# Optimization experiments

Measured on AMD Instinct MI355X. Metric: run time of the kernel, lower is better.

## Reference

```python
import jax, jax.numpy as jnp
import numpy as np

B, NP1, D = 64, 1025, 256  # N+1 tokens, feature dim d (label dim makes d+1)
N_LAYER, N_HEAD = 4, 4
VAR = 0.02


def _pad_pq(allparam):
    """Build padded (d+1)x(d+1) P_full/Q_full for all layers/heads at once.
    P_full gets a 1 at [d, d]; Q_full is zero-padded."""
    L, H, _, d, _ = allparam.shape
    Pf = (jnp.zeros((L, H, d + 1, d + 1), allparam.dtype)
          .at[:, :, :d, :d].set(allparam[:, :, 0])
          .at[:, :, d, d].set(1.0))
    Qf = (jnp.zeros((L, H, d + 1, d + 1), allparam.dtype)
          .at[:, :, :d, :d].set(allparam[:, :, 1]))
    return Pf, Qf


def setup_inputs() -> dict:
    key = jax.random.key(0)
    k1, k2 = jax.random.split(key)
    Z = jax.random.normal(k1, (B, NP1, D + 1), dtype=jnp.float32)
    allparam = jax.random.normal(k2, (N_LAYER, N_HEAD, 2, D, D), dtype=jnp.float32) * VAR
    return {"Z": Z, "allparam": allparam}


def reference(Z, allparam):
    Bb, Np1, dp1 = Z.shape
    N = Np1 - 1
    Pf, Qf = _pad_pq(allparam)  # (L, H, d+1, d+1)
    # mask A = diag(1,...,1,0): equivalent to zeroing the last key token
    mask = jnp.ones((Np1,), Z.dtype).at[N].set(0.0)
    for l in range(allparam.shape[0]):
        # attn[b,h,n,m] = Z[b,n,:] @ Q_full[h] @ Z[b,m,:]
        attn = jnp.einsum('bni,hij,bmj->bhnm', Z, Qf[l], Z)
        attn = jax.nn.relu(attn)
        # key[b,h,m,i] = P_full[h] @ Z[b,m,:], last token masked out (A matrix)
        key_t = jnp.einsum('hij,bmj->bhmi', Pf[l], Z) * mask[None, None, :, None]
        # sum over heads fused into the einsum reduction; scale by 1/N
        res = jnp.einsum('bhnm,bhmi->bni', attn, key_t) / N
        Z = Z + res  # residual connection
    return Z
```

## Files before the change

### kernel.cpp

```cpp
#include <hip/hip_runtime.h>
#include <cstdint>
#include <cstddef>

#define B_    64
#define NP1   1025
#define N_    1024
#define D_    256
#define DP1   257
#define L_    4
#define H_    4
#define MT    1024
#define NCHE  32
#define IPAD  272
#define TR_   1024

typedef __bf16 bf16;
typedef bf16 bf16x4 __attribute__((ext_vector_type(4)));
typedef bf16 bf16x8 __attribute__((ext_vector_type(8)));
typedef float f32x4 __attribute__((ext_vector_type(4)));

__device__ __forceinline__ f32x4 mfma16(bf16x8 a, bf16x8 b, f32x4 c) {
    return __builtin_amdgcn_mfma_f32_16x16x32_bf16(a, b, c, 0, 0, 0);
}

__device__ __forceinline__ void async16(const void* g, void* l) {
    __builtin_amdgcn_global_load_lds(
        (const __attribute__((address_space(1))) void*)g,
        (__attribute__((address_space(3))) void*)l, 16, 0, 0);
}

__global__ void k_prep_pq(const float* __restrict__ ap,
                          bf16* __restrict__ Pb, bf16* __restrict__ Qt) {
    int idx = blockIdx.x * 256 + threadIdx.x;
    int j  = idx & 255;
    int i  = (idx >> 8) & 255;
    int lh = idx >> 16;
    const float* base = ap + (size_t)lh * 2 * D_ * D_;
    float p = base[i * D_ + j];
    float q = base[D_ * D_ + i * D_ + j];
    Pb[((size_t)lh * D_ + i) * D_ + j] = (bf16)p;
    Qt[((size_t)lh * D_ + j) * D_ + i] = (bf16)q;
}

__global__ __launch_bounds__(256) void k_zbt(const float* __restrict__ Z,
                                             bf16* __restrict__ Zb,
                                             bf16* __restrict__ ZbT) {
    __shared__ float t[64][65];
    int m0 = blockIdx.x * 64, j0 = blockIdx.y * 64, b = blockIdx.z;
    int c = threadIdx.x & 63, r0 = threadIdx.x >> 6;
#pragma unroll
    for (int s = 0; s < 16; s++) {
        int r = s * 4 + r0;
        int j = j0 + c;
        float v = (j < DP1) ? Z[((size_t)b * NP1 + m0 + r) * DP1 + j] : 0.f;
        t[r][c] = v;
        if (j < D_) Zb[((size_t)b * N_ + m0 + r) * D_ + j] = (bf16)v;
    }
    __syncthreads();
#pragma unroll
    for (int s = 0; s < 16; s++) {
        int rr = s * 4 + r0;
        int j = j0 + rr;
        if (j < DP1)
            ZbT[((size_t)b * DP1 + j) * MT + m0 + c] = (bf16)t[c][rr];
    }
}

__global__ __launch_bounds__(512, 1) void k_attn(const bf16* __restrict__ Zb,
                                                 const bf16* __restrict__ ZbT,
                                                 const bf16* __restrict__ Qt,
                                                 const bf16* __restrict__ Pb,
                                                 float* __restrict__ Z,
                                                 bf16* __restrict__ T,
                                                 bf16* __restrict__ Tlab,
                                                 int layer) {
    __shared__ bf16 zbS[2][32][256];
    __shared__ bf16 ztS[2][IPAD][32];
    __shared__ bf16 sl[8][32][40];

    const int tid  = threadIdx.x;
    const int id   = blockIdx.x;
    const int wave = tid >> 6, lane = tid & 63;
    const int quad = lane >> 4, l16 = lane & 15;

    if (id >= 256) {
        const int bq = id - 256;
        float* lz1 = (float*)&zbS[0][0][0];
        float* lzq = lz1 + 256;
        float* lsS = lzq + 256;
        float* lT  = lsS + 1024;
        const bf16* Zbb2  = Zb  + (size_t)bq * N_ * D_;
        const bf16* ZbTb2 = ZbT + (size_t)bq * DP1 * MT;
        if (tid < 256) lz1[tid] = Z[((size_t)bq * NP1 + N_) * DP1 + tid];
        float outacc = 0.f, labacc = 0.f;
        __syncthreads();
        for (int h = 0; h < H_; h++) {
            const bf16* Qth = Qt + (size_t)(layer * H_ + h) * D_ * D_;
            const bf16* Ph  = Pb + (size_t)(layer * H_ + h) * D_ * D_;
            if (tid < 256) {
                float a = 0.f;
                const bf16* qr = Qth + (size_t)tid * D_;
                for (int i8 = 0; i8 < 32; i8++) {
                    bf16x8 q = *(const bf16x8*)(qr + i8 * 8);
#pragma unroll
                    for (int k = 0; k < 8; k++) a += lz1[i8 * 8 + k] * (float)q[k];
                }
                lzq[tid] = a;
            }
            __syncthreads();
            for (int m = tid; m < N_; m += 512) {
                float a = 0.f;
                const bf16* zr = Zbb2 + (size_t)m * D_;
                for (int j8 = 0; j8 < 32; j8++) {
                    bf16x8 z8 = *(const bf16x8*)(zr + j8 * 8);
#pragma unroll
                    for (int k = 0; k < 8; k++) a += lzq[j8 * 8 + k] * (float)z8[k];
                }
                lsS[m] = a > 0.f ? a : 0.f;
            }
            __syncthreads();
            if (tid < DP1) {
                float tv = 0.f;
                const bf16* tr2 = ZbTb2 + (size_t)tid * MT;
                for (int m8 = 0; m8 < 128; m8++) {
                    bf16x8 t8 = *(const bf16x8*)(tr2 + m8 * 8);
#pragma unroll
                    for (int k = 0; k < 8; k++) tv += lsS[m8 * 8 + k] * (float)t8[k];
                }
                lT[tid] = tv;
            }
            __syncthreads();
            if (tid < 256) {
                const bf16* pr = Ph + (size_t)tid * D_;
                for (int j8 = 0; j8 < 32; j8++) {
                    bf16x8 p8 = *(const bf16x8*)(pr + j8 * 8);
#pragma unroll
                    for (int k = 0; k < 8; k++) outacc += lT[j8 * 8 + k] * (float)p8[k];
                }
            } else if (tid == 256) {
                labacc += lT[256];
            }
            __syncthreads();
        }
        const float inv = 1.0f / (float)N_;
        if (tid < 256)  Z[((size_t)bq * NP1 + N_) * DP1 + tid] += outacc * inv;
        if (tid == 256) Z[((size_t)bq * NP1 + N_) * DP1 + D_]  += labacc * inv;
        return;
    }

    const int xcd = id & 7, u = id >> 3;
    const int b   = xcd + 8 * (u & 7);
    const int bx  = u >> 3;
    const int n0w = bx * 256 + wave * 32;

    const bf16* Zbb  = Zb  + (size_t)b * N_ * D_;
    const bf16* ZbTb = ZbT + (size_t)b * DP1 * MT;

    const int zrow  = wave * 2 + (lane >> 5);
    const int zscol = ((lane & 31) ^ (zrow & 7)) * 8;
    const int krow  = wave * 16 + (lane >> 2);
    const int kscol = ((lane & 3) ^ ((lane >> 3) & 3)) * 8;
    const int xs    = l16 & 7;
    const int kf    = (l16 >> 1) & 3;

    auto stage = [&](int mc_, int p_) {
        int m0 = mc_ * 32;
        const bf16* zsrc = Zbb + (size_t)(m0 + zrow) * D_ + zscol;
#pragma unroll
        for (int t = 0; t < 2; t++)
            async16(zsrc + (size_t)t * 16 * D_, &zbS[p_][t * 16 + wave * 2][0]);
        const bf16* ksrc = ZbTb + (size_t)krow * MT + m0 + kscol;
#pragma unroll
        for (int t = 0; t < 2; t++)
            async16(ksrc + (size_t)t * 128 * MT, &ztS[p_][t * 128 + wave * 16][0]);
        if (wave == 0)
            async16(ksrc + (size_t)256 * MT, &ztS[p_][256][0]);
    };

    int p = 0;

    for (int h = 0; h < H_; h++) {
        const bf16* Qth = Qt + (size_t)(layer * H_ + h) * D_ * D_;

        if (h == 0) stage(0, 0);

        f32x4 acc[2][17];
#pragma unroll
        for (int ns = 0; ns < 2; ns++)
#pragma unroll
            for (int it = 0; it < 17; it++) acc[ns][it] = (f32x4){0.f, 0.f, 0.f, 0.f};

        bf16x8 zqa[2][8];
#pragma unroll 2
        for (int jc = 0; jc < 8; jc++) {
            f32x4 c00 = (f32x4){0.f,0.f,0.f,0.f}, c01 = c00, c10 = c00, c11 = c00;
#pragma unroll
            for (int kc = 0; kc < 8; kc++) {
                const bf16* qb = Qth + (size_t)(jc * 32 + l16) * D_ + kc * 32 + quad * 8;
                const bf16* az = Zbb + (size_t)(n0w + l16) * D_ + kc * 32 + quad * 8;
                bf16x8 q0 = *(const bf16x8*)(qb);
                bf16x8 q1 = *(const bf16x8*)(qb + 16 * D_);
                bf16x8 a0 = *(const bf16x8*)(az);
                bf16x8 a1 = *(const bf16x8*)(az + 16 * D_);
                c00 = mfma16(q0, a0, c00);
                c01 = mfma16(q0, a1, c01);
                c10 = mfma16(q1, a0, c10);
                c11 = mfma16(q1, a1, c11);
            }
            f32x4 cv[2][2] = {{c00, c01}, {c10, c11}};
#pragma unroll
            for (int jt = 0; jt < 2; jt++)
#pragma unroll
                for (int ns = 0; ns < 2; ns++) {
                    bf16x4 pk;
#pragma unroll
                    for (int r = 0; r < 4; r++) pk[r] = (bf16)cv[jt][ns][r];
                    *(bf16x4*)(&sl[wave][ns * 16 + l16][jt * 16 + quad * 4]) = pk;
                }
#pragma unroll
            for (int ns = 0; ns < 2; ns++)
                zqa[ns][jc] = *(const bf16x8*)(&sl[wave][ns * 16 + l16][quad * 8]);
        }

        if (h == 0) {
            asm volatile("s_waitcnt vmcnt(0)" ::: "memory");
            __builtin_amdgcn_s_barrier();
            __builtin_amdgcn_sched_barrier(0);
        }

        for (int cc = 0; cc < NCHE; cc++) {
            const bool haveNext = (cc + 1 < NCHE);
            if (haveNext) {
                int mcn = (h & 1) ? (NCHE - 2 - cc) : (cc + 1);
                stage(mcn, p ^ 1);
                if (wave == 0) asm volatile("s_waitcnt vmcnt(5)" ::: "memory");
                else           asm volatile("s_waitcnt vmcnt(4)" ::: "memory");
            } else {
                asm volatile("s_waitcnt vmcnt(0)" ::: "memory");
            }
            __builtin_amdgcn_s_barrier();
            __builtin_amdgcn_sched_barrier(0);

#pragma unroll
            for (int mt = 0; mt < 2; mt++) {
                f32x4 st0 = (f32x4){0.f,0.f,0.f,0.f}, st1 = st0;
                const bf16* zr = &zbS[p][mt * 16 + l16][0];
                __builtin_amdgcn_s_setprio(1);
#pragma unroll
                for (int kc = 0; kc < 8; kc++) {
                    bf16x8 az = *(const bf16x8*)(zr + (((kc * 4 + quad) ^ xs) * 8));
                    st0 = mfma16(az, zqa[0][kc], st0);
                    st1 = mfma16(az, zqa[1][kc], st1);
                }
                __builtin_amdgcn_s_setprio(0);
                bf16x4 p0, p1;
#pragma unroll
                for (int r = 0; r < 4; r++) {
                    p0[r] = (bf16)(st0[r] > 0.f ? st0[r] : 0.f);
                    p1[r] = (bf16)(st1[r] > 0.f ? st1[r] : 0.f);
                }
                *(bf16x4*)(&sl[wave][l16][mt * 16 + quad * 4])      = p0;
                *(bf16x4*)(&sl[wave][16 + l16][mt * 16 + quad * 4]) = p1;
            }
            bf16x8 sfrag[2];
#pragma unroll
            for (int ns = 0; ns < 2; ns++)
                sfrag[ns] = *(const bf16x8*)(&sl[wave][ns * 16 + l16][quad * 8]);

            __builtin_amdgcn_s_setprio(1);
#pragma unroll
            for (int it = 0; it < 17; it++) {
                const bf16* kr = &ztS[p][it * 16 + l16][0];
                bf16x8 bk = *(const bf16x8*)(kr + ((quad ^ kf) * 8));
                acc[0][it] = mfma16(sfrag[0], bk, acc[0][it]);
                acc[1][it] = mfma16(sfrag[1], bk, acc[1][it]);
            }
            __builtin_amdgcn_s_setprio(0);

            __builtin_amdgcn_sched_barrier(0);
            __builtin_amdgcn_s_barrier();
            if (haveNext) p ^= 1;
        }

        bf16* Th  = T    + (size_t)(b * H_ + h) * TR_ * D_;
        bf16* Tlh = Tlab + (size_t)(b * H_ + h) * TR_;
#pragma unroll
        for (int ns = 0; ns < 2; ns++)
#pragma unroll
            for (int it = 0; it < 17; it++)
#pragma unroll
                for (int r = 0; r < 4; r++) {
                    int n = n0w + ns * 16 + quad * 4 + r;
                    float v = acc[ns][it][r];
                    if (it < 16)
                        Th[(size_t)n * D_ + it * 16 + l16] = (bf16)v;
                    else if (l16 == 0)
                        Tlh[n] = (bf16)v;
                }
    }
}

__global__ __launch_bounds__(256, 4) void k_post(const bf16* __restrict__ T,
                                                 const bf16* __restrict__ Tlab,
                                                 const bf16* __restrict__ Pb,
                                                 float* __restrict__ Z,
                                                 bf16* __restrict__ Zb,
                                                 bf16* __restrict__ ZbT,
                                                 int layer) {
    const int tid  = threadIdx.x;
    const int id   = blockIdx.x;
    const int wave = tid >> 6, lane = tid & 63;
    const int quad = lane >> 4, l16 = lane & 15;
    const int xcd = id & 7, u = id >> 3;
    const int b   = xcd + 8 * (u & 3) + 32 * ((u >> 5) & 1);
    const int bx  = (u >> 2) & 7;
    const int ih  = u >> 6;
    const int n0w = bx * 128 + wave * 32;
    const int i0  = ih * 128;

    f32x4 acc[2][8];
#pragma unroll
    for (int ns = 0; ns < 2; ns++)
#pragma unroll
        for (int it = 0; it < 8; it++) acc[ns][it] = (f32x4){0.f, 0.f, 0.f, 0.f};

    for (int h = 0; h < H_; h++) {
        const bf16* Th = T  + (size_t)(b * H_ + h) * TR_ * D_;
        const bf16* Ph = Pb + (size_t)(layer * H_ + h) * D_ * D_;
#pragma unroll 2
        for (int kc = 0; kc < 8; kc++) {
            bf16x8 af[2];
#pragma unroll
            for (int ns = 0; ns < 2; ns++) {
                int row = n0w + ns * 16 + l16;
                af[ns] = *(const bf16x8*)(Th + (size_t)row * D_ + kc * 32 + quad * 8);
            }
#pragma unroll
            for (int it = 0; it < 8; it++) {
                bf16x8 bp = *(const bf16x8*)(Ph + (size_t)(i0 + it * 16 + l16) * D_ + kc * 32 + quad * 8);
                acc[0][it] = mfma16(af[0], bp, acc[0][it]);
                acc[1][it] = mfma16(af[1], bp, acc[1][it]);
            }
        }
    }

    const float inv = 1.0f / (float)N_;
    const bool wnext = (layer < L_ - 1);
#pragma unroll
    for (int ns = 0; ns < 2; ns++)
#pragma unroll
        for (int it = 0; it < 8; it++) {
            const int i = i0 + it * 16 + l16;
            const int nbase = n0w + ns * 16 + quad * 4;
            bf16x4 zpk;
#pragma unroll
            for (int r = 0; r < 4; r++) {
                int n = nbase + r;
                size_t zi = ((size_t)b * NP1 + n) * DP1 + i;
                float v = Z[zi] + acc[ns][it][r] * inv;
                Z[zi] = v;
                zpk[r] = (bf16)v;
                if (wnext) Zb[((size_t)b * N_ + n) * D_ + i] = (bf16)v;
            }
            if (wnext)
                *(bf16x4*)(&ZbT[((size_t)b * DP1 + i) * MT + nbase]) = zpk;
        }
    if (ih == 0 && tid < 128) {
        int n = bx * 128 + tid;
        float s = 0.f;
#pragma unroll
        for (int h = 0; h < H_; h++)
            s += (float)Tlab[(size_t)(b * H_ + h) * TR_ + n];
        size_t zi = ((size_t)b * NP1 + n) * DP1 + D_;
        float v = Z[zi] + s * inv;
        Z[zi] = v;
        if (wnext) ZbT[((size_t)b * DP1 + D_) * MT + n] = (bf16)v;
    }
}

extern "C" void kernel_launch(void* const* d_in, const int* in_sizes, int n_in,
                              void* d_out, int out_size, void* d_ws, size_t ws_size,
                              hipStream_t stream) {
    const float* Zin = (const float*)d_in[0];
    const float* ap  = (const float*)d_in[1];
    float* Z = (float*)d_out;

    char* ws = (char*)d_ws;
    const size_t sz_Zb  = (size_t)B_ * N_ * D_ * sizeof(bf16);
    const size_t sz_ZbT = (size_t)B_ * DP1 * MT * sizeof(bf16);
    const size_t sz_T   = (size_t)B_ * H_ * TR_ * D_ * sizeof(bf16);
    const size_t sz_Tl  = (size_t)B_ * H_ * TR_ * sizeof(bf16);
    const size_t sz_P   = (size_t)L_ * H_ * D_ * D_ * sizeof(bf16);
    bf16* Zb  = (bf16*)ws;
    bf16* ZbT = (bf16*)(ws + sz_Zb);
    bf16* Tb  = (bf16*)(ws + sz_Zb + sz_ZbT);
    bf16* Tl  = (bf16*)(ws + sz_Zb + sz_ZbT + sz_T);
    bf16* Pb  = (bf16*)(ws + sz_Zb + sz_ZbT + sz_T + sz_Tl);
    bf16* Qt  = (bf16*)(ws + sz_Zb + sz_ZbT + sz_T + sz_Tl + sz_P);

    hipMemcpyAsync(Z, Zin, (size_t)B_ * NP1 * DP1 * sizeof(float),
                   hipMemcpyDeviceToDevice, stream);

    k_prep_pq<<<dim3((L_ * H_ * D_ * D_) / 256), 256, 0, stream>>>(ap, Pb, Qt);
    k_zbt<<<dim3(N_ / 64, 5, B_), 256, 0, stream>>>(Z, Zb, ZbT);

    for (int l = 0; l < L_; l++) {
        k_attn<<<dim3(320), 512, 0, stream>>>(Zb, ZbT, Qt, Pb, Z, Tb, Tl, l);
        k_post<<<dim3(1024), 256, 0, stream>>>(Tb, Tl, Pb, Z, Zb, ZbT, l);
    }
}
```

Measured before the change: 3.590 ms.

## Fold last-token query work into main attention blocks and batch heads

```diff
diff --git a/kernel.cpp b/kernel.cpp
--- a/kernel.cpp
+++ b/kernel.cpp
@@ -83,71 +83,6 @@
     const int wave = tid >> 6, lane = tid & 63;
     const int quad = lane >> 4, l16 = lane & 15;
 
-    if (id >= 256) {
-        const int bq = id - 256;
-        float* lz1 = (float*)&zbS[0][0][0];
-        float* lzq = lz1 + 256;
-        float* lsS = lzq + 256;
-        float* lT  = lsS + 1024;
-        const bf16* Zbb2  = Zb  + (size_t)bq * N_ * D_;
-        const bf16* ZbTb2 = ZbT + (size_t)bq * DP1 * MT;
-        if (tid < 256) lz1[tid] = Z[((size_t)bq * NP1 + N_) * DP1 + tid];
-        float outacc = 0.f, labacc = 0.f;
-        __syncthreads();
-        for (int h = 0; h < H_; h++) {
-            const bf16* Qth = Qt + (size_t)(layer * H_ + h) * D_ * D_;
-            const bf16* Ph  = Pb + (size_t)(layer * H_ + h) * D_ * D_;
-            if (tid < 256) {
-                float a = 0.f;
-                const bf16* qr = Qth + (size_t)tid * D_;
-                for (int i8 = 0; i8 < 32; i8++) {
-                    bf16x8 q = *(const bf16x8*)(qr + i8 * 8);
-#pragma unroll
-                    for (int k = 0; k < 8; k++) a += lz1[i8 * 8 + k] * (float)q[k];
-                }
-                lzq[tid] = a;
-            }
-            __syncthreads();
-            for (int m = tid; m < N_; m += 512) {
-                float a = 0.f;
-                const bf16* zr = Zbb2 + (size_t)m * D_;
-                for (int j8 = 0; j8 < 32; j8++) {
-                    bf16x8 z8 = *(const bf16x8*)(zr + j8 * 8);
-#pragma unroll
-                    for (int k = 0; k < 8; k++) a += lzq[j8 * 8 + k] * (float)z8[k];
-                }
-                lsS[m] = a > 0.f ? a : 0.f;
-            }
-            __syncthreads();
-            if (tid < DP1) {
-                float tv = 0.f;
-                const bf16* tr2 = ZbTb2 + (size_t)tid * MT;
-                for (int m8 = 0; m8 < 128; m8++) {
-                    bf16x8 t8 = *(const bf16x8*)(tr2 + m8 * 8);
-#pragma unroll
-                    for (int k = 0; k < 8; k++) tv += lsS[m8 * 8 + k] * (float)t8[k];
-                }
-                lT[tid] = tv;
-            }
-            __syncthreads();
-            if (tid < 256) {
-                const bf16* pr = Ph + (size_t)tid * D_;
-                for (int j8 = 0; j8 < 32; j8++) {
-                    bf16x8 p8 = *(const bf16x8*)(pr + j8 * 8);
-#pragma unroll
-                    for (int k = 0; k < 8; k++) outacc += lT[j8 * 8 + k] * (float)p8[k];
-                }
-            } else if (tid == 256) {
-                labacc += lT[256];
-            }
-            __syncthreads();
-        }
-        const float inv = 1.0f / (float)N_;
-        if (tid < 256)  Z[((size_t)bq * NP1 + N_) * DP1 + tid] += outacc * inv;
-        if (tid == 256) Z[((size_t)bq * NP1 + N_) * DP1 + D_]  += labacc * inv;
-        return;
-    }
-
     const int xcd = id & 7, u = id >> 3;
     const int b   = xcd + 8 * (u & 7);
     const int bx  = u >> 3;
@@ -297,6 +232,86 @@
                     else if (l16 == 0)
                         Tlh[n] = (bf16)v;
                 }
+    }
+
+    if (bx == 0) {
+        __syncthreads();
+        float* lz1 = (float*)&zbS[0][0][0];
+        float* lzq = lz1 + 256;
+        float* lsS = lzq + 1024;
+        float* lT  = lsS + 4096;
+        if (tid < 256) lz1[tid] = Z[((size_t)b * NP1 + N_) * DP1 + tid];
+        __syncthreads();
+        {
+            int j = tid & 255, hh = tid >> 8;
+            for (int h2 = hh; h2 < H_; h2 += 2) {
+                const bf16* qr = Qt + ((size_t)(layer * H_ + h2) * D_ + j) * D_;
+                float a = 0.f;
+                for (int i8 = 0; i8 < 32; i8++) {
+                    bf16x8 q = *(const bf16x8*)(qr + i8 * 8);
+#pragma unroll
+                    for (int k = 0; k < 8; k++) a += lz1[i8 * 8 + k] * (float)q[k];
+                }
+                lzq[h2 * 256 + j] = a;
+            }
+        }
+        __syncthreads();
+        for (int m = tid; m < N_; m += 512) {
+            const bf16* zr = Zbb + (size_t)m * D_;
+            float a0 = 0.f, a1 = 0.f, a2 = 0.f, a3 = 0.f;
+            for (int j8 = 0; j8 < 32; j8++) {
+                bf16x8 z8 = *(const bf16x8*)(zr + j8 * 8);
+#pragma unroll
+                for (int k = 0; k < 8; k++) {
+                    float zv = (float)z8[k];
+                    int j = j8 * 8 + k;
+                    a0 += lzq[j] * zv;
+                    a1 += lzq[256 + j] * zv;
+                    a2 += lzq[512 + j] * zv;
+                    a3 += lzq[768 + j] * zv;
+                }
+            }
+            lsS[m]        = a0 > 0.f ? a0 : 0.f;
+            lsS[1024 + m] = a1 > 0.f ? a1 : 0.f;
+            lsS[2048 + m] = a2 > 0.f ? a2 : 0.f;
+            lsS[3072 + m] = a3 > 0.f ? a3 : 0.f;
+        }
+        __syncthreads();
+        if (tid < DP1) {
+            const bf16* tr2 = ZbTb + (size_t)tid * MT;
+            float t0 = 0.f, t1 = 0.f, t2 = 0.f, t3 = 0.f;
+            for (int m8 = 0; m8 < 128; m8++) {
+                bf16x8 t8 = *(const bf16x8*)(tr2 + m8 * 8);
+#pragma unroll
+                for (int k = 0; k < 8; k++) {
+                    float zv = (float)t8[k];
+                    int m = m8 * 8 + k;
+                    t0 += lsS[m] * zv;
+                    t1 += lsS[1024 + m] * zv;
+                    t2 += lsS[2048 + m] * zv;
+                    t3 += lsS[3072 + m] * zv;
+                }
+            }
+            lT[tid] = t0; lT[257 + tid] = t1; lT[514 + tid] = t2; lT[771 + tid] = t3;
+        }
+        __syncthreads();
+        const float inv = 1.0f / (float)N_;
+        if (tid < 256) {
+            float out = 0.f;
+            for (int h2 = 0; h2 < H_; h2++) {
+                const bf16* pr = Pb + ((size_t)(layer * H_ + h2) * D_ + tid) * D_;
+                for (int j8 = 0; j8 < 32; j8++) {
+                    bf16x8 p8 = *(const bf16x8*)(pr + j8 * 8);
+#pragma unroll
+                    for (int k = 0; k < 8; k++)
+                        out += lT[h2 * 257 + j8 * 8 + k] * (float)p8[k];
+                }
+            }
+            Z[((size_t)b * NP1 + N_) * DP1 + tid] += out * inv;
+        } else if (tid == 256) {
+            float lab = lT[256] + lT[513] + lT[770] + lT[1027];
+            Z[((size_t)b * NP1 + N_) * DP1 + D_] += lab * inv;
+        }
     }
 }
 
@@ -405,7 +420,7 @@
     k_zbt<<<dim3(N_ / 64, 5, B_), 256, 0, stream>>>(Z, Zb, ZbT);
 
     for (int l = 0; l < L_; l++) {
-        k_attn<<<dim3(320), 512, 0, stream>>>(Zb, ZbT, Qt, Pb, Z, Tb, Tl, l);
+        k_attn<<<dim3(256), 512, 0, stream>>>(Zb, ZbT, Qt, Pb, Z, Tb, Tl, l);
         k_post<<<dim3(1024), 256, 0, stream>>>(Tb, Tl, Pb, Z, Zb, ZbT, l);
     }
 }
```

Measured after the change: 3.326 ms. 7.4% less time.
